# Optimization experiments

Hardware: AMD Instinct MI355X
Metric: run time of the kernel (lower is better)

The kernel has to match this reference:

```python
import jax, jax.numpy as jnp
import numpy as np

B, N, C = 128, 320, 768
H = 12
T = 64    # template tokens (8x8)
S = 256   # search tokens (16x16)


def setup_inputs() -> dict:
    key = jax.random.key(0)
    k1, k2, k3, k4 = jax.random.split(key, 4)
    return {
        "x1": jax.random.normal(k1, (B, N, C), dtype=jnp.float32),
        "x2": jax.random.normal(k2, (B, N, C), dtype=jnp.float32),
        "qkv_w": jax.random.normal(k3, (3 * C, C), dtype=jnp.float32) * 0.02,
        "proj_w": jax.random.normal(k4, (C, C), dtype=jnp.float32) * 0.02,
        "proj_b": jnp.zeros((C,), dtype=jnp.float32),
    }


def reference(x1, x2, qkv_w, proj_w, proj_b):
    # concat template tokens from x1 with search tokens from x2
    x = jnp.concatenate([x1[:, :T, :], x2[:, T:, :]], axis=1)  # [B, N, C]
    b, n, c = x.shape
    d = c // H
    scale = d ** -0.5

    qkv = (x @ qkv_w.T).reshape(b, n, 3, H, d).transpose(2, 0, 3, 1, 4)  # [3,B,H,N,D]
    q, k, v = qkv[0], qkv[1], qkv[2]

    # template -> template self-attention
    q_mt, k_mt, v_mt = q[:, :, :T], k[:, :, :T], v[:, :, :T]
    attn_mt = jax.nn.softmax(jnp.einsum('bhtd,bhsd->bhts', q_mt, k_mt) * scale, axis=-1)
    x_mt = jnp.einsum('bhts,bhsd->bhtd', attn_mt, v_mt).transpose(0, 2, 1, 3).reshape(b, T, c)

    # search -> all cross+self attention
    q_s = q[:, :, T:]
    attn_s = jax.nn.softmax(jnp.einsum('bhqd,bhkd->bhqk', q_s, k) * scale, axis=-1)
    x_s = jnp.einsum('bhqk,bhkd->bhqd', attn_s, v).transpose(0, 2, 1, 3).reshape(b, S, c)

    out = jnp.concatenate([x_mt, x_s], axis=1) @ proj_w.T + proj_b
    return out
```

## Files before the change

### kernel.cpp

```cpp
#include <hip/hip_runtime.h>
#include <hip/hip_bf16.h>
#include <stdint.h>

#define B_   128
#define N_   320
#define C_   768
#define H_   12
#define D_   64
#define NT_  (B_*N_)
#define K3_  (3*C_)
#define NKT  12
#define TE   (256*64)

typedef __attribute__((ext_vector_type(8))) __bf16 bf16x8;
typedef __attribute__((ext_vector_type(4))) float  f32x4;

__device__ __forceinline__ unsigned short f2bf(float f) {
  union { float f; unsigned u; } v; v.f = f;
  return (unsigned short)((v.u + 0x7fffu + ((v.u >> 16) & 1u)) >> 16);
}

__device__ __forceinline__ void gload16(const unsigned short* g, unsigned short* l) {
  __builtin_amdgcn_global_load_lds((const __attribute__((address_space(1))) void*)g,
                                   (__attribute__((address_space(3))) void*)l,
                                   16, 0, 0);
}

__global__ void prep_x(const float* __restrict__ x1, const float* __restrict__ x2,
                       unsigned short* __restrict__ xb) {
  const unsigned total4 = (unsigned)NT_ * C_ / 4;
  const unsigned stride = gridDim.x * blockDim.x;
  for (unsigned i = blockIdx.x * blockDim.x + threadIdx.x; i < total4; i += stride) {
    unsigned tok = i / (C_ / 4);
    unsigned n   = tok % N_;
    const float* src = (n < 64u) ? x1 : x2;
    float4 v = *(const float4*)(src + (size_t)i * 4u);
    ushort4 o;
    o.x = f2bf(v.x); o.y = f2bf(v.y); o.z = f2bf(v.z); o.w = f2bf(v.w);
    *(ushort4*)(xb + (size_t)i * 4u) = o;
  }
}

__global__ void prep_w(const float* __restrict__ qkv_w, const float* __restrict__ proj_w,
                       unsigned short* __restrict__ wq, unsigned short* __restrict__ wp) {
  const int QKV4 = (K3_ * C_) / 4;
  const int Q4   = (C_ * C_) / 4;
  const int P4   = (C_ * C_) / 4;
  int i = blockIdx.x * 256 + threadIdx.x;
  if (i < QKV4) {
    float s = (i < Q4) ? 0.125f : 1.0f;
    float4 v = *(const float4*)(qkv_w + (size_t)i * 4);
    ushort4 o;
    o.x = f2bf(v.x * s); o.y = f2bf(v.y * s); o.z = f2bf(v.z * s); o.w = f2bf(v.w * s);
    *(ushort4*)(wq + (size_t)i * 4) = o;
  } else if (i < QKV4 + P4) {
    int j = i - QKV4;
    float4 v = *(const float4*)(proj_w + (size_t)j * 4);
    ushort4 o;
    o.x = f2bf(v.x); o.y = f2bf(v.y); o.z = f2bf(v.z); o.w = f2bf(v.w);
    *(ushort4*)(wp + (size_t)j * 4) = o;
  }
}

#define BARR do { asm volatile("" ::: "memory"); __builtin_amdgcn_s_barrier(); asm volatile("" ::: "memory"); } while(0)
#define DSW  asm volatile("s_waitcnt lgkmcnt(0)" ::: "memory")
#define VMW(n) asm volatile("s_waitcnt vmcnt(" #n ")" ::: "memory")
#define PRIO1 __builtin_amdgcn_s_setprio(1)
#define PRIO0 __builtin_amdgcn_s_setprio(0)
#define RD(base, off) (*(const bf16x8*)((base) + (off)))

#define LDA_Q(ARR, QQ, PARX) do { \
    ARR[0][0] = RD(bAk0, (PARX)*32768 + (QQ)*8192);        \
    ARR[0][1] = RD(bAk1, (PARX)*32768 + (QQ)*8192);        \
    ARR[1][0] = RD(bAk0, (PARX)*32768 + (QQ)*8192 + 2048); \
    ARR[1][1] = RD(bAk1, (PARX)*32768 + (QQ)*8192 + 2048); } while(0)

#define LDB(PARX) do { \
    _Pragma("unroll") for (int nf = 0; nf < 4; ++nf) { \
      b_[0][nf] = RD(bBk0, (PARX)*32768 + nf*2048); \
      b_[1][nf] = RD(bBk1, (PARX)*32768 + nf*2048); } } while(0)

#define MFN(ARR, QQ) do { \
    _Pragma("unroll") for (int ks = 0; ks < 2; ++ks) \
    _Pragma("unroll") for (int f = 0; f < 2; ++f) \
    _Pragma("unroll") for (int nf = 0; nf < 4; ++nf) \
      acc[(QQ)*2+f][nf] = __builtin_amdgcn_mfma_f32_16x16x32_bf16(ARR[f][ks], b_[ks][nf], acc[(QQ)*2+f][nf], 0, 0, 0); \
  } while(0)

#define MFS(ARR, QQ) do { \
    _Pragma("unroll") for (int ks = 0; ks < 2; ++ks) \
    _Pragma("unroll") for (int f = 0; f < 2; ++f) \
    _Pragma("unroll") for (int nf = 0; nf < 4; ++nf) \
      acc[(QQ)*2+f][nf] = __builtin_amdgcn_mfma_f32_16x16x32_bf16(b_[ks][nf], ARR[f][ks], acc[(QQ)*2+f][nf], 0, 0, 0); \
  } while(0)

#define STGA4(PARX) do { \
    gload16(gA00, dA + ((PARX)^1)*TE);        gload16(gA01, dA + ((PARX)^1)*TE + 512);  \
    gload16(gA10, dA + ((PARX)^1)*TE + 8192); gload16(gA11, dA + ((PARX)^1)*TE + 8704); \
    gA00 += 64; gA01 += 64; gA10 += 64; gA11 += 64; } while(0)
#define STGB4(PARX) do { \
    gload16(gB00, dB + (PARX)*TE);        gload16(gB01, dB + (PARX)*TE + 512);  \
    gload16(gB10, dB + (PARX)*TE + 8192); gload16(gB11, dB + (PARX)*TE + 8704); \
    gB00 += 64; gB01 += 64; gB10 += 64; gB11 += 64; } while(0)

#define KT2(MF, PARX, S0_, S1_) do { \
    LDA_Q(aL_, 0, PARX); LDA_Q(aH_, 1, PARX); LDB(PARX); S0_; \
    DSW; PRIO1; MF(aL_, 0); MF(aH_, 1); PRIO0; BARR; \
    LDA_Q(aL_, 2, PARX); LDA_Q(aH_, 3, PARX); S1_; \
    DSW; PRIO1; MF(aL_, 2); MF(aH_, 3); PRIO0; VMW(4); BARR; \
  } while(0)

#define RESETA do { \
    gA00 = Ag_ + (size_t)row0n*768 + offA00; gA01 = Ag_ + (size_t)row0n*768 + offA01; \
    gA10 = Ag_ + (size_t)row0n*768 + offA10; gA11 = Ag_ + (size_t)row0n*768 + offA11; } while(0)
#define RESETB do { \
    gB00 = Wg_ + (size_t)col0n*768 + offA00; gB01 = Wg_ + (size_t)col0n*768 + offA01; \
    gB10 = Wg_ + (size_t)col0n*768 + offA10; gB11 = Wg_ + (size_t)col0n*768 + offA11; } while(0)

#define TILE12(MF) do { \
    _Pragma("unroll 1") for (int tt = 0; tt < 5; ++tt) { \
      KT2(MF, 0, STGA4(0), STGB4(0)); \
      KT2(MF, 1, STGA4(1), STGB4(1)); \
    } \
    KT2(MF, 0, STGA4(0), { RESETB; STGB4(0); }); \
    KT2(MF, 1, { RESETA; STGA4(1); }, STGB4(1)); \
  } while(0)

#define GEMM_SETUP \
  const int tid = threadIdx.x, lane = tid & 63, w = tid >> 6; \
  const int wr = w >> 2, wc = w & 3; \
  const int lr = lane & 15, kg = lane >> 4; \
  const int rr = lane >> 3; \
  const int sp = (lane & 7) ^ rr; \
  const char* bAk0 = (const char*)As + wr*4096 + lr*128 + ((0*4 + kg) ^ (lr & 7))*16; \
  const char* bAk1 = (const char*)As + wr*4096 + lr*128 + ((1*4 + kg) ^ (lr & 7))*16; \
  const char* bBk0 = (const char*)Bs + wc*8192 + lr*128 + ((0*4 + kg) ^ (lr & 7))*16; \
  const char* bBk1 = (const char*)Bs + wc*8192 + lr*128 + ((1*4 + kg) ^ (lr & 7))*16; \
  const size_t offA00 = (size_t)(w*16 + rr)*768 + sp*8; \
  const size_t offA01 = offA00 + (size_t)8*768; \
  const size_t offA10 = offA00 + (size_t)128*768; \
  const size_t offA11 = offA01 + (size_t)128*768; \
  unsigned short* dA = As + w*1024; \
  unsigned short* dB = Bs + w*1024; \
  const unsigned short *gA00, *gA01, *gA10, *gA11, *gB00, *gB01, *gB10, *gB11;

#define GEMM_PROLOGUE(row0i, col0i) do { \
    gA00 = Ag_ + (size_t)(row0i)*768 + offA00 + 64;  gA01 = Ag_ + (size_t)(row0i)*768 + offA01 + 64; \
    gA10 = Ag_ + (size_t)(row0i)*768 + offA10 + 64;  gA11 = Ag_ + (size_t)(row0i)*768 + offA11 + 64; \
    gB00 = Wg_ + (size_t)(col0i)*768 + offA00 + 128; gB01 = Wg_ + (size_t)(col0i)*768 + offA01 + 128; \
    gB10 = Wg_ + (size_t)(col0i)*768 + offA10 + 128; gB11 = Wg_ + (size_t)(col0i)*768 + offA11 + 128; \
    gload16(gA00 - 64,  dA);              gload16(gA01 - 64,  dA + 512); \
    gload16(gA10 - 64,  dA + 8192);       gload16(gA11 - 64,  dA + 8704); \
    gload16(gB00 - 128, dB);              gload16(gB01 - 128, dB + 512); \
    gload16(gB10 - 128, dB + 8192);       gload16(gB11 - 128, dB + 8704); \
    gload16(gB00 - 64,  dB + TE);         gload16(gB01 - 64,  dB + TE + 512); \
    gload16(gB10 - 64,  dB + TE + 8192);  gload16(gB11 - 64,  dB + TE + 8704); \
    VMW(4); BARR; \
  } while(0)

#define ACC_ZERO do { \
    _Pragma("unroll") for (int mf = 0; mf < 8; ++mf) \
    _Pragma("unroll") for (int nf = 0; nf < 4; ++nf) acc[mf][nf] = vzero; } while(0)

__global__ void __launch_bounds__(512) gemm_qkv(const unsigned short* __restrict__ A,
                                                const unsigned short* __restrict__ W,
                                                unsigned short* __restrict__ qb,
                                                unsigned short* __restrict__ kb,
                                                unsigned short* __restrict__ vb) {
  __shared__ __align__(16) unsigned short As[2 * TE];
  __shared__ __align__(16) unsigned short Bs[2 * TE];
  GEMM_SETUP
  const unsigned short* Ag_ = A;
  const unsigned short* Wg_ = W;
  const int wv = blockIdx.x / 80;
  const int lb = blockIdx.x - wv * 80;

  const f32x4 vzero = {0.f, 0.f, 0.f, 0.f};
  f32x4 acc[8][4];
  ACC_ZERO;
  bf16x8 aL_[2][2], aH_[2][2], b_[2][4];

  {
    const int t0i = lb * 6;
    const int row0i = (t0i / 3) * 256, col0i = (wv * 3 + t0i % 3) * 256;
    GEMM_PROLOGUE(row0i, col0i);
  }

  if (wv != 2) {
    unsigned short* dst = (wv == 0) ? qb : kb;
#pragma unroll 1
    for (int j = 0; j < 6; ++j) {
      const int t = lb * 6 + j, tn = (j < 5) ? t + 1 : t;
      const int row0c = (t / 3) * 256, cb = (t % 3) * 256;
      const int row0n = (tn / 3) * 256, col0n = (wv * 3 + tn % 3) * 256;
      TILE12(MFS);
#pragma unroll
      for (int mf = 0; mf < 8; ++mf) {
        const int tok = row0c + (mf >> 1) * 64 + wr * 32 + (mf & 1) * 16 + lr;
        const unsigned bq = (unsigned)tok / 320u;
        const int tt2 = tok - (int)bq * 320;
#pragma unroll
        for (int nf = 0; nf < 4; ++nf) {
          const int nn = cb + wc * 64 + nf * 16 + kg * 4;
          const int h = nn >> 6, dd = nn & 63;
          ushort4 o;
          o.x = f2bf(acc[mf][nf][0]); o.y = f2bf(acc[mf][nf][1]);
          o.z = f2bf(acc[mf][nf][2]); o.w = f2bf(acc[mf][nf][3]);
          *(ushort4*)&dst[(size_t)((((int)bq * 12 + h) * 320 + tt2) * 64 + dd)] = o;
        }
      }
      ACC_ZERO;
    }
  } else {
#pragma unroll 1
    for (int j = 0; j < 6; ++j) {
      const int t = lb * 6 + j, tn = (j < 5) ? t + 1 : t;
      const int row0c = (t / 3) * 256, cb = (t % 3) * 256;
      const int row0n = (tn / 3) * 256, col0n = (wv * 3 + tn % 3) * 256;
      TILE12(MFN);
#pragma unroll
      for (int mf = 0; mf < 8; ++mf) {
        const int m0 = row0c + (mf >> 1) * 64 + wr * 32 + (mf & 1) * 16 + kg * 4;
        const unsigned bq = (unsigned)m0 / 320u;
        const int t0v = m0 - (int)bq * 320;
#pragma unroll
        for (int nf = 0; nf < 4; ++nf) {
          const int nn = cb + wc * 64 + nf * 16 + lr;
          const int h = nn >> 6, dd = nn & 63;
          ushort4 o;
          o.x = f2bf(acc[mf][nf][0]); o.y = f2bf(acc[mf][nf][1]);
          o.z = f2bf(acc[mf][nf][2]); o.w = f2bf(acc[mf][nf][3]);
          *(ushort4*)&vb[(size_t)(((((int)bq * 12 + h) * 64 + dd) * 320) + t0v)] = o;
        }
      }
      ACC_ZERO;
    }
  }
  asm volatile("s_waitcnt vmcnt(0) lgkmcnt(0)" ::: "memory");
}

__global__ void __launch_bounds__(256) attn(const unsigned short* __restrict__ qb,
                                            const unsigned short* __restrict__ kb,
                                            const unsigned short* __restrict__ vb,
                                            unsigned short* __restrict__ ab) {
  __shared__ __align__(16) unsigned short Ks[64 * 64];
  __shared__ __align__(16) unsigned short Vt[64 * 64];
  __shared__ __align__(16) unsigned short Pl[4 * 16 * 64];
  const int bid = blockIdx.x;
  const int qt = bid % 5, bh = bid / 5;
  const int tid = threadIdx.x, lane = tid & 63, w = tid >> 6;
  const int lr = lane & 15, kg = lane >> 4;

  const int qrow = qt * 64 + w * 16 + lr;
  const unsigned short* qptr = qb + (bh * 320 + qrow) * 64;
  const bf16x8 qa0 = *(const bf16x8*)(qptr + kg * 8);
  const bf16x8 qa1 = *(const bf16x8*)(qptr + 32 + kg * 8);

  f32x4 o[4] = {};
  float mrun[4] = {-1e30f, -1e30f, -1e30f, -1e30f};
  float lrun[4] = {0.f, 0.f, 0.f, 0.f};
  const int nchunk = (qt == 0) ? 1 : 5;

  const int c0 = w, c1 = w + 4;
  const int srow0 = c0 * 8 + (lane >> 3);
  const int srow1 = c1 * 8 + (lane >> 3);
  const int slot  = lane & 7;
  const int part0 = slot ^ (srow0 & 7);
  const int part1 = slot ^ (srow1 & 7);
  const unsigned short* kbase = kb + bh * 320 * 64;
  const unsigned short* vbase = vb + bh * 64 * 320;
  unsigned short* lk0 = &Ks[c0 * 512];
  unsigned short* lk1 = &Ks[c1 * 512];
  unsigned short* lv0 = &Vt[c0 * 512];
  unsigned short* lv1 = &Vt[c1 * 512];
  char* PwB = (char*)&Pl[w * 1024];

  for (int kc = 0; kc < nchunk; kc++) {
    gload16(kbase + (kc * 64 + srow0) * 64 + part0 * 8, lk0);
    gload16(kbase + (kc * 64 + srow1) * 64 + part1 * 8, lk1);
    gload16(vbase + srow0 * 320 + kc * 64 + part0 * 8, lv0);
    gload16(vbase + srow1 * 320 + kc * 64 + part1 * 8, lv1);
    __syncthreads();

    f32x4 s[4];
#pragma unroll
    for (int kt = 0; kt < 4; kt++) {
      const int key = kt * 16 + lr;
      const char* kr = (const char*)Ks + key * 128;
      const unsigned sw = (unsigned)((key & 7) << 4);
      bf16x8 k0 = *(const bf16x8*)(kr + ((kg * 16) ^ sw));
      bf16x8 k1 = *(const bf16x8*)(kr + ((64 + kg * 16) ^ sw));
      f32x4 z = {0.f, 0.f, 0.f, 0.f};
      z = __builtin_amdgcn_mfma_f32_16x16x32_bf16(qa0, k0, z, 0, 0, 0);
      z = __builtin_amdgcn_mfma_f32_16x16x32_bf16(qa1, k1, z, 0, 0, 0);
      s[kt] = z;
    }

#pragma unroll
    for (int r = 0; r < 4; r++) {
      float rm = fmaxf(fmaxf(s[0][r], s[1][r]), fmaxf(s[2][r], s[3][r]));
      rm = fmaxf(rm, __shfl_xor(rm, 1));
      rm = fmaxf(rm, __shfl_xor(rm, 2));
      rm = fmaxf(rm, __shfl_xor(rm, 4));
      rm = fmaxf(rm, __shfl_xor(rm, 8));
      const float mn = fmaxf(mrun[r], rm);
      const float alpha = __expf(mrun[r] - mn);
      mrun[r] = mn;
      const int q = kg * 4 + r;
      char* prow = PwB + q * 128;
      const unsigned sw = (unsigned)((q & 7) << 4);
      float rs = 0.f;
#pragma unroll
      for (int kt = 0; kt < 4; kt++) {
        const float p = __expf(s[kt][r] - mn);
        rs += p;
        const int key = kt * 16 + lr;
        *(unsigned short*)(prow + ((key * 2) ^ sw)) = f2bf(p);
      }
      rs += __shfl_xor(rs, 1);
      rs += __shfl_xor(rs, 2);
      rs += __shfl_xor(rs, 4);
      rs += __shfl_xor(rs, 8);
      lrun[r] = lrun[r] * alpha + rs;
#pragma unroll
      for (int dt = 0; dt < 4; dt++) o[dt][r] *= alpha;
    }

    asm volatile("s_waitcnt lgkmcnt(0)" ::: "memory");

    {
      const char* par = (const char*)PwB + lr * 128;
      const unsigned swp = (unsigned)((lr & 7) << 4);
      bf16x8 p0 = *(const bf16x8*)(par + ((kg * 16) ^ swp));
      bf16x8 p1 = *(const bf16x8*)(par + ((64 + kg * 16) ^ swp));
#pragma unroll
      for (int dt = 0; dt < 4; dt++) {
        const int d = dt * 16 + lr;
        const char* vr = (const char*)Vt + d * 128;
        const unsigned swv = (unsigned)((d & 7) << 4);
        bf16x8 v0 = *(const bf16x8*)(vr + ((kg * 16) ^ swv));
        bf16x8 v1 = *(const bf16x8*)(vr + ((64 + kg * 16) ^ swv));
        o[dt] = __builtin_amdgcn_mfma_f32_16x16x32_bf16(p0, v0, o[dt], 0, 0, 0);
        o[dt] = __builtin_amdgcn_mfma_f32_16x16x32_bf16(p1, v1, o[dt], 0, 0, 0);
      }
    }
    __syncthreads();
  }

  const int b = bh / 12, h = bh - b * 12;
#pragma unroll
  for (int r = 0; r < 4; r++) {
    const float inv = 1.0f / lrun[r];
    const int token = b * 320 + qt * 64 + w * 16 + kg * 4 + r;
    unsigned short* orow = ab + token * 768 + h * 64;
#pragma unroll
    for (int dt = 0; dt < 4; dt++)
      orow[dt * 16 + lr] = f2bf(o[dt][r] * inv);
  }
}

__global__ void __launch_bounds__(512) gemm_proj(const unsigned short* __restrict__ A,
                                                 const unsigned short* __restrict__ W,
                                                 const float* __restrict__ bias,
                                                 float* __restrict__ out) {
  __shared__ __align__(16) unsigned short As[2 * TE];
  __shared__ __align__(16) unsigned short Bs[2 * TE];
  GEMM_SETUP
  const unsigned short* Ag_ = A;
  const unsigned short* Wg_ = W;
  const int lb = blockIdx.x;

  const f32x4 vzero = {0.f, 0.f, 0.f, 0.f};
  f32x4 acc[8][4];
  ACC_ZERO;
  bf16x8 aL_[2][2], aH_[2][2], b_[2][4];

  {
    const int t0i = lb * 2;
    const int row0i = (t0i / 3) * 256, col0i = (t0i % 3) * 256;
    GEMM_PROLOGUE(row0i, col0i);
  }

#pragma unroll 1
  for (int j = 0; j < 2; ++j) {
    const int t = lb * 2 + j, tn = (j < 1) ? t + 1 : t;
    const int row0c = (t / 3) * 256, col0c = (t % 3) * 256;
    const int row0n = (tn / 3) * 256, col0n = (tn % 3) * 256;
    TILE12(MFN);
#pragma unroll
    for (int nf = 0; nf < 4; ++nf) {
      const int nn = col0c + wc * 64 + nf * 16 + lr;
      const float bv = bias[nn];
#pragma unroll
      for (int mf = 0; mf < 8; ++mf) {
        const int m0 = row0c + (mf >> 1) * 64 + wr * 32 + (mf & 1) * 16 + kg * 4;
        float* po = out + (size_t)m0 * 768 + nn;
#pragma unroll
        for (int r = 0; r < 4; r++)
          po[(size_t)r * 768] = acc[mf][nf][r] + bv;
      }
    }
    ACC_ZERO;
  }
  asm volatile("s_waitcnt vmcnt(0) lgkmcnt(0)" ::: "memory");
}

extern "C" void kernel_launch(void* const* d_in, const int* in_sizes, int n_in,
                              void* d_out, int out_size, void* d_ws, size_t ws_size,
                              hipStream_t stream) {
  (void)in_sizes; (void)n_in; (void)out_size; (void)ws_size;
  const float* x1     = (const float*)d_in[0];
  const float* x2     = (const float*)d_in[1];
  const float* qkv_w  = (const float*)d_in[2];
  const float* proj_w = (const float*)d_in[3];
  const float* proj_b = (const float*)d_in[4];
  float* out = (float*)d_out;

  const size_t TOK = (size_t)NT_ * C_;
  unsigned short* xb = (unsigned short*)d_ws;
  unsigned short* qb = xb + TOK;
  unsigned short* kb = qb + TOK;
  unsigned short* vb = kb + TOK;
  unsigned short* ab = vb + TOK;
  unsigned short* wq = ab + TOK;
  unsigned short* wp = wq + (size_t)K3_ * C_;

  prep_x<<<8192, 256, 0, stream>>>(x1, x2, xb);
  prep_w<<<2304, 256, 0, stream>>>(qkv_w, proj_w, wq, wp);
  gemm_qkv<<<240, 512, 0, stream>>>(xb, wq, qb, kb, vb);
  attn<<<1536 * 5, 256, 0, stream>>>(qb, kb, vb, ab);
  gemm_proj<<<240, 512, 0, stream>>>(ab, wp, proj_b, out);
}
```

Measured before the change: 406.9 us.

## Restructure GEMM k-loop into single-barrier stage with interleaved LDS reads and MFMAs

Replaces the two-half-step k-tile pipeline, which had staggered A/B staging and two barriers per k-tile, with a uniform double-buffered scheme. A and B are now both prefetched into the other buffer at the start of each k-tile, and LDS fragment reads are interleaved with MFMA groups instead of waiting on lgkmcnt(0). The aim is fewer barriers and better overlap of LDS reads with matrix math. In exchange it waits for all outstanding global loads (vmcnt 0) at the end of every k-tile, which may expose memory latency that the old deeper prefetch hid.

```diff
diff --git a/kernel.cpp b/kernel.cpp
--- a/kernel.cpp
+++ b/kernel.cpp
@@ -63,7 +63,6 @@
 }
 
 #define BARR do { asm volatile("" ::: "memory"); __builtin_amdgcn_s_barrier(); asm volatile("" ::: "memory"); } while(0)
-#define DSW  asm volatile("s_waitcnt lgkmcnt(0)" ::: "memory")
 #define VMW(n) asm volatile("s_waitcnt vmcnt(" #n ")" ::: "memory")
 #define PRIO1 __builtin_amdgcn_s_setprio(1)
 #define PRIO0 __builtin_amdgcn_s_setprio(0)
@@ -99,15 +98,22 @@
     gload16(gA10, dA + ((PARX)^1)*TE + 8192); gload16(gA11, dA + ((PARX)^1)*TE + 8704); \
     gA00 += 64; gA01 += 64; gA10 += 64; gA11 += 64; } while(0)
 #define STGB4(PARX) do { \
-    gload16(gB00, dB + (PARX)*TE);        gload16(gB01, dB + (PARX)*TE + 512);  \
-    gload16(gB10, dB + (PARX)*TE + 8192); gload16(gB11, dB + (PARX)*TE + 8704); \
+    gload16(gB00, dB + ((PARX)^1)*TE);        gload16(gB01, dB + ((PARX)^1)*TE + 512);  \
+    gload16(gB10, dB + ((PARX)^1)*TE + 8192); gload16(gB11, dB + ((PARX)^1)*TE + 8704); \
     gB00 += 64; gB01 += 64; gB10 += 64; gB11 += 64; } while(0)
-
-#define KT2(MF, PARX, S0_, S1_) do { \
-    LDA_Q(aL_, 0, PARX); LDA_Q(aH_, 1, PARX); LDB(PARX); S0_; \
-    DSW; PRIO1; MF(aL_, 0); MF(aH_, 1); PRIO0; BARR; \
-    LDA_Q(aL_, 2, PARX); LDA_Q(aH_, 3, PARX); S1_; \
-    DSW; PRIO1; MF(aL_, 2); MF(aH_, 3); PRIO0; VMW(4); BARR; \
+#define STG8(PARX) do { STGA4(PARX); STGB4(PARX); } while(0)
+
+#define KT1(MF, PARX, STG_) do { \
+    LDB(PARX); LDA_Q(aL_, 0, PARX); \
+    STG_; \
+    LDA_Q(aH_, 1, PARX); \
+    PRIO1; MF(aL_, 0); PRIO0; \
+    LDA_Q(aL_, 2, PARX); \
+    PRIO1; MF(aH_, 1); PRIO0; \
+    LDA_Q(aH_, 3, PARX); \
+    PRIO1; MF(aL_, 2); PRIO0; \
+    PRIO1; MF(aH_, 3); PRIO0; \
+    VMW(0); BARR; \
   } while(0)
 
 #define RESETA do { \
@@ -119,11 +125,11 @@
 
 #define TILE12(MF) do { \
     _Pragma("unroll 1") for (int tt = 0; tt < 5; ++tt) { \
-      KT2(MF, 0, STGA4(0), STGB4(0)); \
-      KT2(MF, 1, STGA4(1), STGB4(1)); \
+      KT1(MF, 0, STG8(0)); \
+      KT1(MF, 1, STG8(1)); \
     } \
-    KT2(MF, 0, STGA4(0), { RESETB; STGB4(0); }); \
-    KT2(MF, 1, { RESETA; STGA4(1); }, STGB4(1)); \
+    KT1(MF, 0, STG8(0)); \
+    KT1(MF, 1, { RESETA; RESETB; STG8(1); }); \
   } while(0)
 
 #define GEMM_SETUP \
@@ -145,17 +151,12 @@
   const unsigned short *gA00, *gA01, *gA10, *gA11, *gB00, *gB01, *gB10, *gB11;
 
 #define GEMM_PROLOGUE(row0i, col0i) do { \
-    gA00 = Ag_ + (size_t)(row0i)*768 + offA00 + 64;  gA01 = Ag_ + (size_t)(row0i)*768 + offA01 + 64; \
-    gA10 = Ag_ + (size_t)(row0i)*768 + offA10 + 64;  gA11 = Ag_ + (size_t)(row0i)*768 + offA11 + 64; \
-    gB00 = Wg_ + (size_t)(col0i)*768 + offA00 + 128; gB01 = Wg_ + (size_t)(col0i)*768 + offA01 + 128; \
-    gB10 = Wg_ + (size_t)(col0i)*768 + offA10 + 128; gB11 = Wg_ + (size_t)(col0i)*768 + offA11 + 128; \
-    gload16(gA00 - 64,  dA);              gload16(gA01 - 64,  dA + 512); \
-    gload16(gA10 - 64,  dA + 8192);       gload16(gA11 - 64,  dA + 8704); \
-    gload16(gB00 - 128, dB);              gload16(gB01 - 128, dB + 512); \
-    gload16(gB10 - 128, dB + 8192);       gload16(gB11 - 128, dB + 8704); \
-    gload16(gB00 - 64,  dB + TE);         gload16(gB01 - 64,  dB + TE + 512); \
-    gload16(gB10 - 64,  dB + TE + 8192);  gload16(gB11 - 64,  dB + TE + 8704); \
-    VMW(4); BARR; \
+    gA00 = Ag_ + (size_t)(row0i)*768 + offA00; gA01 = Ag_ + (size_t)(row0i)*768 + offA01; \
+    gA10 = Ag_ + (size_t)(row0i)*768 + offA10; gA11 = Ag_ + (size_t)(row0i)*768 + offA11; \
+    gB00 = Wg_ + (size_t)(col0i)*768 + offA00; gB01 = Wg_ + (size_t)(col0i)*768 + offA01; \
+    gB10 = Wg_ + (size_t)(col0i)*768 + offA10; gB11 = Wg_ + (size_t)(col0i)*768 + offA11; \
+    STG8(1); \
+    VMW(0); BARR; \
   } while(0)
 
 #define ACC_ZERO do { \
```

Result: no change. 406.7 us (-0.1%).
